# Kernel tuning notes

Hardware: AMD Instinct MI355X
Metric: run time of the kernel (lower is better)

Reference implementation:

```python
import jax, jax.numpy as jnp
import numpy as np

MODEL_DIM = 512
KEY_DIM = 64


def setup_inputs() -> dict:
    key = jax.random.key(0)
    ks = jax.random.split(key, 8)
    B, S = 4, 4096
    scale = 1.0 / np.sqrt(MODEL_DIM)
    return {
        "x1": jax.random.normal(ks[0], (B, S, MODEL_DIM), jnp.float32),
        "x2": jax.random.normal(ks[1], (B, S, MODEL_DIM), jnp.float32),
        "Wq": jax.random.normal(ks[2], (MODEL_DIM, KEY_DIM), jnp.float32) * scale,
        "bq": jnp.zeros((KEY_DIM,), jnp.float32),
        "Wk": jax.random.normal(ks[3], (MODEL_DIM, KEY_DIM), jnp.float32) * scale,
        "bk": jnp.zeros((KEY_DIM,), jnp.float32),
        "Wv": jax.random.normal(ks[4], (MODEL_DIM, KEY_DIM), jnp.float32) * scale,
        "bv": jnp.zeros((KEY_DIM,), jnp.float32),
        "apply_mask": 1,
    }


def reference(x1, x2, Wq, bq, Wk, bk, Wv, bv, apply_mask):
    # Linear + ReLU projections (single head, d_k = d_v = KEY_DIM)
    q = jax.nn.relu(x1 @ Wq + bq)  # [B,S,dk]
    k = jax.nn.relu(x2 @ Wk + bk)  # [B,S,dk]
    v = jax.nn.relu(x2 @ Wv + bv)  # [B,S,dk]
    scores = jnp.einsum("bqd,bkd->bqk", q, k) / jnp.sqrt(jnp.float32(KEY_DIM))
    if apply_mask:
        S = scores.shape[-1]
        causal = jnp.tril(jnp.ones((S, S), dtype=bool))  # keep lower-tri incl. diag
        scores = jnp.where(causal, scores, -jnp.inf)
    attn = jax.nn.softmax(scores, axis=-1)
    return jnp.einsum("bqk,bkd->bqd", attn, v)
```

## Files before the change

kernel.cpp:

```cpp
#include <hip/hip_runtime.h>


typedef __attribute__((ext_vector_type(8))) _Float16 f16x8;
typedef __attribute__((ext_vector_type(4))) float f32x4;
typedef __attribute__((ext_vector_type(8))) unsigned short us8;
typedef __attribute__((ext_vector_type(4))) unsigned short us4;

#define AS1 __attribute__((address_space(1)))
#define AS3 __attribute__((address_space(3)))

__device__ __forceinline__ void gload16(const void* g, void* l) {
  __builtin_amdgcn_global_load_lds((const AS1 unsigned int*)g,
                                   (AS3 unsigned int*)l, 16, 0, 0);
}

__device__ __forceinline__ unsigned short f2h(float f) {
  _Float16 h = (_Float16)f;
  return __builtin_bit_cast(unsigned short, h);
}
__device__ __forceinline__ float h2f(unsigned short u) {
  return (float)__builtin_bit_cast(_Float16, u);
}
__device__ __forceinline__ f16x8 us2h(us8 v) {
  return __builtin_bit_cast(f16x8, v);
}

#define S_LEN 4096
#define NROW 16384
#define CCH 8
#define NPMAX 8

__global__ __launch_bounds__(256) void prep_kernel(
    const float* __restrict__ Wq, const float* __restrict__ Wk,
    const float* __restrict__ Wv, unsigned short* __restrict__ wtT) {
  const int kc = blockIdx.x, p = blockIdx.y;
  const float* __restrict__ W = (p == 0) ? Wq : (p == 1) ? Wk : Wv;
  __shared__ unsigned short T[64][72];
  const int t = threadIdx.x;
#pragma unroll
  for (int i = 0; i < 4; i++) {
    int f = t + 256 * i;
    int kk = f >> 4, c4 = (f & 15) << 2;
    float4 v4 = *(const float4*)&W[(size_t)(kc * 64 + kk) * 64 + c4];
    T[c4 + 0][kk] = f2h(v4.x);
    T[c4 + 1][kk] = f2h(v4.y);
    T[c4 + 2][kk] = f2h(v4.z);
    T[c4 + 3][kk] = f2h(v4.w);
  }
  __syncthreads();
  const int n = t >> 2, q4 = (t & 3) << 4;
  us8 o0, o1;
#pragma unroll
  for (int e = 0; e < 8; e++) o0[e] = T[n][q4 + e];
#pragma unroll
  for (int e = 0; e < 8; e++) o1[e] = T[n][q4 + 8 + e];
  unsigned short* dst = &wtT[((size_t)p * 64 + n) * 512 + kc * 64 + q4];
  *(us8*)&dst[0] = o0;
  *(us8*)&dst[8] = o1;
}

__global__ __launch_bounds__(128) void proj_kernel(
    const float* __restrict__ x1, const float* __restrict__ x2,
    const unsigned short* __restrict__ wtT, const float* __restrict__ bq,
    const float* __restrict__ bk, const float* __restrict__ bv,
    unsigned short* __restrict__ qo, unsigned short* __restrict__ ko,
    unsigned short* __restrict__ vto) {
  const int kind = blockIdx.y;
  const float* __restrict__ X = kind ? x2 : x1;
  const int row0 = blockIdx.x * 32;

  __shared__ __align__(16) float XB[2][32 * 64];

  const int t = threadIdx.x, ln = t & 63, w = t >> 6, lm = ln & 15, lg = ln >> 4;

  f32x4 acc0[4], acc1[4];
#pragma unroll
  for (int nt = 0; nt < 4; nt++)
#pragma unroll
    for (int e = 0; e < 4; e++) { acc0[nt][e] = 0.0f; acc1[nt][e] = 0.0f; }

  const unsigned short* __restrict__ wt0 =
      wtT + (size_t)(kind ? 1 : 0) * 64 * 512;
  const unsigned short* __restrict__ wt1 = wtT + (size_t)2 * 64 * 512;

  auto STAGE = [&](int kc, int bi) {
#pragma unroll
    for (int cc = 0; cc < 4; cc++) {
      int c = 4 * w + cc;
      int r = 4 * c + (ln >> 4);
      int s = ln & 15;
      int sg = (s & 8) | ((s & 7) ^ (r & 7));
      gload16(&X[(size_t)(row0 + r) * 512 + kc * 64 + sg * 4],
              &XB[bi][c * 256]);
    }
  };

  STAGE(0, 0);
  for (int kc = 0; kc < 8; kc++) {
    const int bi = kc & 1;
    us8 B0[8], B1[8];
#pragma unroll
    for (int nt = 0; nt < 4; nt++)
#pragma unroll
      for (int h = 0; h < 2; h++)
        B0[nt * 2 + h] = *(const us8*)&wt0[(size_t)(16 * nt + lm) * 512 +
                                           kc * 64 + 32 * h + 8 * lg];
    if (kind) {
#pragma unroll
      for (int nt = 0; nt < 4; nt++)
#pragma unroll
        for (int h = 0; h < 2; h++)
          B1[nt * 2 + h] = *(const us8*)&wt1[(size_t)(16 * nt + lm) * 512 +
                                             kc * 64 + 32 * h + 8 * lg];
    }
    if (kc < 7) STAGE(kc + 1, bi ^ 1);
    if (kind) {
      if (kc < 7) asm volatile("s_waitcnt vmcnt(20)" ::: "memory");
      else        asm volatile("s_waitcnt vmcnt(16)" ::: "memory");
    } else {
      if (kc < 7) asm volatile("s_waitcnt vmcnt(12)" ::: "memory");
      else        asm volatile("s_waitcnt vmcnt(8)" ::: "memory");
    }
    __builtin_amdgcn_sched_barrier(0);
    __builtin_amdgcn_s_barrier();

    const int R = 16 * w + lm;
    f16x8 af[2];
#pragma unroll
    for (int g = 0; g < 2; g++) {
      int sl0 = 8 * g + ((2 * lg) ^ (lm & 7));
      int sl1 = 8 * g + ((2 * lg + 1) ^ (lm & 7));
      f32x4 a0 = *(const f32x4*)&XB[bi][R * 64 + sl0 * 4];
      f32x4 a1 = *(const f32x4*)&XB[bi][R * 64 + sl1 * 4];
      f16x8 v;
      v[0] = (_Float16)a0[0]; v[1] = (_Float16)a0[1];
      v[2] = (_Float16)a0[2]; v[3] = (_Float16)a0[3];
      v[4] = (_Float16)a1[0]; v[5] = (_Float16)a1[1];
      v[6] = (_Float16)a1[2]; v[7] = (_Float16)a1[3];
      af[g] = v;
    }
#pragma unroll
    for (int nt = 0; nt < 4; nt++) {
      acc0[nt] = __builtin_amdgcn_mfma_f32_16x16x32_f16(af[0], us2h(B0[nt * 2 + 0]), acc0[nt], 0, 0, 0);
      acc0[nt] = __builtin_amdgcn_mfma_f32_16x16x32_f16(af[1], us2h(B0[nt * 2 + 1]), acc0[nt], 0, 0, 0);
      if (kind) {
        acc1[nt] = __builtin_amdgcn_mfma_f32_16x16x32_f16(af[0], us2h(B1[nt * 2 + 0]), acc1[nt], 0, 0, 0);
        acc1[nt] = __builtin_amdgcn_mfma_f32_16x16x32_f16(af[1], us2h(B1[nt * 2 + 1]), acc1[nt], 0, 0, 0);
      }
    }
    __builtin_amdgcn_sched_barrier(0);
    __builtin_amdgcn_s_barrier();
  }

  if (kind == 0) {
#pragma unroll
    for (int nt = 0; nt < 4; nt++)
#pragma unroll
      for (int r = 0; r < 4; r++) {
        int row = row0 + 16 * w + 4 * lg + r;
        int col = 16 * nt + lm;
        float v = fmaxf(acc0[nt][r] + bq[col], 0.0f) * 0.125f;
        qo[(size_t)row * 64 + col] = f2h(v);
      }
  } else {
#pragma unroll
    for (int nt = 0; nt < 4; nt++)
#pragma unroll
      for (int r = 0; r < 4; r++) {
        int row = row0 + 16 * w + 4 * lg + r;
        int col = 16 * nt + lm;
        float v = fmaxf(acc0[nt][r] + bk[col], 0.0f);
        ko[(size_t)row * 64 + col] = f2h(v);
      }
    unsigned short* TB = (unsigned short*)&XB[0][0];
#pragma unroll
    for (int nt = 0; nt < 4; nt++)
#pragma unroll
      for (int r = 0; r < 4; r++) {
        float v = fmaxf(acc1[nt][r] + bv[16 * nt + lm], 0.0f);
        TB[(16 * w + 4 * lg + r) * 72 + 16 * nt + lm] = f2h(v);
      }
    __syncthreads();
    const int d = t >> 1, s0 = (t & 1) << 4;
    us8 o0, o1;
#pragma unroll
    for (int e = 0; e < 8; e++) o0[e] = TB[(s0 + e) * 72 + d];
#pragma unroll
    for (int e = 0; e < 8; e++) o1[e] = TB[(s0 + 8 + e) * 72 + d];
    const int batch = row0 >> 12, sl = row0 & 4095;
    unsigned short* vp = &vto[((size_t)batch * 64 + d) * S_LEN + sl + s0];
    *(us8*)&vp[0] = o0;
    *(us8*)&vp[8] = o1;
  }
}

__global__ __launch_bounds__(256) void attn_part(
    const unsigned short* __restrict__ q, const unsigned short* __restrict__ k,
    const unsigned short* __restrict__ vT, const int* __restrict__ amask,
    unsigned short* __restrict__ pO, float* __restrict__ pml) {
  const int qt = blockIdx.x, j = blockIdx.y, b = blockIdx.z;
  const int mask = *amask;
  const int sb = j * CCH;
  if (mask && sb > qt) return;
  const int se0 = sb + CCH - 1;
  const int se = mask ? ((qt < se0) ? qt : se0) : se0;

  const int t = threadIdx.x, ln = t & 63, w = t >> 6, lm = ln & 15, lg = ln >> 4;

  __shared__ __align__(16) unsigned short KB[2][4096];
  __shared__ __align__(16) unsigned short VB[2][4096];
  __shared__ __align__(16) unsigned short Ps[4][16][72];

  const unsigned short* __restrict__ qb = q + (size_t)b * S_LEN * 64;
  const unsigned short* __restrict__ kb = k + (size_t)b * S_LEN * 64;
  const unsigned short* __restrict__ vb = vT + (size_t)b * 64 * S_LEN;

  const size_t qoff = (size_t)(qt * 64 + 16 * w + lm) * 64;
  f16x8 qf0 = *(const f16x8*)&qb[qoff + 8 * lg];
  f16x8 qf1 = *(const f16x8*)&qb[qoff + 32 + 8 * lg];

  const int rr = ln >> 3;
  const int sg = (ln & 7) ^ (rr & 7);
  auto STAGE = [&](int s, int bi) {
    const int kv0 = s * 64;
#pragma unroll
    for (int cc = 0; cc < 2; cc++) {
      int c = 2 * w + cc;
      int r = 8 * c + rr;
      gload16(&kb[(size_t)(kv0 + r) * 64 + sg * 8], &KB[bi][c * 512]);
      gload16(&vb[(size_t)r * S_LEN + kv0 + sg * 8], &VB[bi][c * 512]);
    }
  };

  f32x4 accO[4];
#pragma unroll
  for (int dt = 0; dt < 4; dt++)
#pragma unroll
    for (int e = 0; e < 4; e++) accO[dt][e] = 0.0f;
  float m0 = -1e30f, l0 = 0.0f;

  const int sx = lm & 7;
  STAGE(sb, 0);
  for (int s = sb; s <= se; s++) {
    const int bi = (s - sb) & 1;
    if (s < se) {
      STAGE(s + 1, bi ^ 1);
      asm volatile("s_waitcnt vmcnt(4)" ::: "memory");
    } else {
      asm volatile("s_waitcnt vmcnt(0)" ::: "memory");
    }
    __builtin_amdgcn_sched_barrier(0);
    __builtin_amdgcn_s_barrier();

    f32x4 sc[4];
#pragma unroll
    for (int nt = 0; nt < 4; nt++) {
#pragma unroll
      for (int e = 0; e < 4; e++) sc[nt][e] = 0.0f;
      const int R = 16 * nt + lm;
      f16x8 kf0 = *(const f16x8*)&KB[bi][R * 64 + (lg ^ sx) * 8];
      f16x8 kf1 = *(const f16x8*)&KB[bi][R * 64 + ((4 + lg) ^ sx) * 8];
      sc[nt] = __builtin_amdgcn_mfma_f32_16x16x32_f16(kf0, qf0, sc[nt], 0, 0, 0);
      sc[nt] = __builtin_amdgcn_mfma_f32_16x16x32_f16(kf1, qf1, sc[nt], 0, 0, 0);
    }

    if (mask && s == qt) {
#pragma unroll
      for (int nt = 0; nt < 4; nt++)
#pragma unroll
        for (int r = 0; r < 4; r++)
          if (16 * nt + 4 * lg + r > 16 * w + lm) sc[nt][r] = -1e30f;
    }

    float mx = fmaxf(fmaxf(fmaxf(sc[0][0], sc[0][1]), fmaxf(sc[0][2], sc[0][3])),
                     fmaxf(fmaxf(sc[1][0], sc[1][1]), fmaxf(sc[1][2], sc[1][3])));
    float mx2 = fmaxf(fmaxf(fmaxf(sc[2][0], sc[2][1]), fmaxf(sc[2][2], sc[2][3])),
                      fmaxf(fmaxf(sc[3][0], sc[3][1]), fmaxf(sc[3][2], sc[3][3])));
    mx = fmaxf(mx, mx2);
    mx = fmaxf(mx, __shfl_xor(mx, 16));
    mx = fmaxf(mx, __shfl_xor(mx, 32));
    const float mn = fmaxf(m0, mx);
    const float fs = __expf(m0 - mn);
    m0 = mn;

    float pv[4][4];
    float su = 0.0f;
#pragma unroll
    for (int nt = 0; nt < 4; nt++)
#pragma unroll
      for (int r = 0; r < 4; r++) {
        pv[nt][r] = __expf(sc[nt][r] - mn);
        su += pv[nt][r];
      }
    su += __shfl_xor(su, 16);
    su += __shfl_xor(su, 32);
    l0 = l0 * fs + su;
#pragma unroll
    for (int dt = 0; dt < 4; dt++)
#pragma unroll
      for (int e = 0; e < 4; e++) accO[dt][e] *= fs;

#pragma unroll
    for (int nt = 0; nt < 4; nt++) {
      us4 w4;
#pragma unroll
      for (int r = 0; r < 4; r++) w4[r] = f2h(pv[nt][r]);
      *(us4*)&Ps[w][lm][16 * nt + 4 * lg] = w4;
    }

    f16x8 pf0 = *(const f16x8*)&Ps[w][lm][8 * lg];
    f16x8 pf1 = *(const f16x8*)&Ps[w][lm][32 + 8 * lg];
#pragma unroll
    for (int dt = 0; dt < 4; dt++) {
      const int R = 16 * dt + lm;
      f16x8 vf0 = *(const f16x8*)&VB[bi][R * 64 + (lg ^ sx) * 8];
      f16x8 vf1 = *(const f16x8*)&VB[bi][R * 64 + ((4 + lg) ^ sx) * 8];
      accO[dt] = __builtin_amdgcn_mfma_f32_16x16x32_f16(vf0, pf0, accO[dt], 0, 0, 0);
      accO[dt] = __builtin_amdgcn_mfma_f32_16x16x32_f16(vf1, pf1, accO[dt], 0, 0, 0);
    }
    __builtin_amdgcn_sched_barrier(0);
    __builtin_amdgcn_s_barrier();
  }

  const size_t ub = (size_t)(b * 64 + qt) * NPMAX + j;
  unsigned short* __restrict__ Op = pO + ub * 4096;
#pragma unroll
  for (int dt = 0; dt < 4; dt++) {
    us4 o4;
#pragma unroll
    for (int r = 0; r < 4; r++) o4[r] = f2h(accO[dt][r]);
    *(us4*)&Op[(16 * w + lm) * 64 + 16 * dt + 4 * lg] = o4;
  }
  if (lg == 0) {
    float* __restrict__ mlp = pml + ub * 128;
    mlp[(16 * w + lm) * 2 + 0] = m0;
    mlp[(16 * w + lm) * 2 + 1] = l0;
  }
}

__global__ __launch_bounds__(256) void combine_kernel(
    const unsigned short* __restrict__ pO, const float* __restrict__ pml,
    const int* __restrict__ amask, float* __restrict__ out) {
  const int qt = blockIdx.x, cg = blockIdx.y, b = blockIdx.z;
  const int mask = *amask;
  const int np = mask ? (qt / CCH + 1) : NPMAX;
  const int t = threadIdx.x;
  const int row = t >> 2, c = ((t & 3) << 2) + (cg << 4);
  const size_t base = (size_t)(b * 64 + qt) * NPMAX;

  float M = -1e30f;
  for (int jj = 0; jj < np; jj++)
    M = fmaxf(M, pml[(base + jj) * 128 + row * 2]);

  float L = 0.0f;
  float a[4] = {0.f, 0.f, 0.f, 0.f};
  for (int jj = 0; jj < np; jj++) {
    const float* mlp = &pml[(base + jj) * 128 + row * 2];
    float wj = __expf(mlp[0] - M);
    L += mlp[1] * wj;
    us4 h = *(const us4*)&pO[(base + jj) * 4096 + row * 64 + c];
#pragma unroll
    for (int e = 0; e < 4; e++) a[e] += wj * h2f(h[e]);
  }
  const float inv = 1.0f / L;
  f32x4 o;
#pragma unroll
  for (int e = 0; e < 4; e++) o[e] = a[e] * inv;
  *(f32x4*)&out[((size_t)b * S_LEN + qt * 64 + row) * 64 + c] = o;
}

extern "C" void kernel_launch(void* const* d_in, const int* in_sizes, int n_in,
                              void* d_out, int out_size, void* d_ws, size_t ws_size,
                              hipStream_t stream) {
  const float* x1 = (const float*)d_in[0];
  const float* x2 = (const float*)d_in[1];
  const float* Wq = (const float*)d_in[2];
  const float* bq = (const float*)d_in[3];
  const float* Wk = (const float*)d_in[4];
  const float* bk = (const float*)d_in[5];
  const float* Wv = (const float*)d_in[6];
  const float* bv = (const float*)d_in[7];
  const int* amask = (const int*)d_in[8];

  unsigned short* qws = (unsigned short*)d_ws;
  unsigned short* kws = qws + (size_t)NROW * 64;
  unsigned short* vtws = kws + (size_t)NROW * 64;
  unsigned short* wtT = vtws + (size_t)NROW * 64;
  unsigned short* pO = wtT + (size_t)3 * 64 * 512;
  float* pml = (float*)(pO + (size_t)2048 * 4096);
  float* out = (float*)d_out;

  prep_kernel<<<dim3(8, 3), 256, 0, stream>>>(Wq, Wk, Wv, wtT);
  proj_kernel<<<dim3(512, 2), 128, 0, stream>>>(x1, x2, wtT, bq, bk, bv,
                                                qws, kws, vtws);
  attn_part<<<dim3(64, NPMAX, 4), 256, 0, stream>>>(qws, kws, vtws, amask,
                                                    pO, pml);
  combine_kernel<<<dim3(64, 4, 4), 256, 0, stream>>>(pO, pml, amask, out);
}
```

Measured before the change: 165.7 us.

## Load projection inputs directly to registers and raise MFMA wave priority in attention

The projection kernel no longer stages X tiles through double-buffered LDS with async global_load_lds, explicit vmcnt waits and barriers. Each lane now reads its own row of X directly from global memory into registers, and weight fragments are loaded inline next to their MFMAs. This removes the LDS footprint and the block-wide syncs, at the cost of less latency hiding and possibly less coalesced global reads. Separately, the attention kernel wraps its QK and PV MFMA blocks in s_setprio(1) so those waves are favoured by the scheduler.

```diff
diff --git a/kernel.cpp b/kernel.cpp
--- a/kernel.cpp
+++ b/kernel.cpp
@@ -69,7 +69,7 @@
   const float* __restrict__ X = kind ? x2 : x1;
   const int row0 = blockIdx.x * 32;
 
-  __shared__ __align__(16) float XB[2][32 * 64];
+  __shared__ __align__(16) unsigned short TB[32 * 72];
 
   const int t = threadIdx.x, ln = t & 63, w = t >> 6, lm = ln & 15, lg = ln >> 4;
 
@@ -82,74 +82,37 @@
   const unsigned short* __restrict__ wt0 =
       wtT + (size_t)(kind ? 1 : 0) * 64 * 512;
   const unsigned short* __restrict__ wt1 = wtT + (size_t)2 * 64 * 512;
-
-  auto STAGE = [&](int kc, int bi) {
-#pragma unroll
-    for (int cc = 0; cc < 4; cc++) {
-      int c = 4 * w + cc;
-      int r = 4 * c + (ln >> 4);
-      int s = ln & 15;
-      int sg = (s & 8) | ((s & 7) ^ (r & 7));
-      gload16(&X[(size_t)(row0 + r) * 512 + kc * 64 + sg * 4],
-              &XB[bi][c * 256]);
-    }
-  };
-
-  STAGE(0, 0);
+  const float* __restrict__ xrow = &X[(size_t)(row0 + 16 * w + lm) * 512];
+
+#pragma unroll 2
   for (int kc = 0; kc < 8; kc++) {
-    const int bi = kc & 1;
-    us8 B0[8], B1[8];
-#pragma unroll
-    for (int nt = 0; nt < 4; nt++)
-#pragma unroll
-      for (int h = 0; h < 2; h++)
-        B0[nt * 2 + h] = *(const us8*)&wt0[(size_t)(16 * nt + lm) * 512 +
-                                           kc * 64 + 32 * h + 8 * lg];
-    if (kind) {
-#pragma unroll
-      for (int nt = 0; nt < 4; nt++)
-#pragma unroll
-        for (int h = 0; h < 2; h++)
-          B1[nt * 2 + h] = *(const us8*)&wt1[(size_t)(16 * nt + lm) * 512 +
-                                             kc * 64 + 32 * h + 8 * lg];
-    }
-    if (kc < 7) STAGE(kc + 1, bi ^ 1);
-    if (kind) {
-      if (kc < 7) asm volatile("s_waitcnt vmcnt(20)" ::: "memory");
-      else        asm volatile("s_waitcnt vmcnt(16)" ::: "memory");
-    } else {
-      if (kc < 7) asm volatile("s_waitcnt vmcnt(12)" ::: "memory");
-      else        asm volatile("s_waitcnt vmcnt(8)" ::: "memory");
-    }
-    __builtin_amdgcn_sched_barrier(0);
-    __builtin_amdgcn_s_barrier();
-
-    const int R = 16 * w + lm;
     f16x8 af[2];
 #pragma unroll
-    for (int g = 0; g < 2; g++) {
-      int sl0 = 8 * g + ((2 * lg) ^ (lm & 7));
-      int sl1 = 8 * g + ((2 * lg + 1) ^ (lm & 7));
-      f32x4 a0 = *(const f32x4*)&XB[bi][R * 64 + sl0 * 4];
-      f32x4 a1 = *(const f32x4*)&XB[bi][R * 64 + sl1 * 4];
+    for (int h = 0; h < 2; h++) {
+      const float* ap = &xrow[kc * 64 + 32 * h + 8 * lg];
+      float4 a0 = *(const float4*)ap;
+      float4 a1 = *(const float4*)(ap + 4);
       f16x8 v;
-      v[0] = (_Float16)a0[0]; v[1] = (_Float16)a0[1];
-      v[2] = (_Float16)a0[2]; v[3] = (_Float16)a0[3];
-      v[4] = (_Float16)a1[0]; v[5] = (_Float16)a1[1];
-      v[6] = (_Float16)a1[2]; v[7] = (_Float16)a1[3];
-      af[g] = v;
+      v[0] = (_Float16)a0.x; v[1] = (_Float16)a0.y;
+      v[2] = (_Float16)a0.z; v[3] = (_Float16)a0.w;
+      v[4] = (_Float16)a1.x; v[5] = (_Float16)a1.y;
+      v[6] = (_Float16)a1.z; v[7] = (_Float16)a1.w;
+      af[h] = v;
     }
 #pragma unroll
     for (int nt = 0; nt < 4; nt++) {
-      acc0[nt] = __builtin_amdgcn_mfma_f32_16x16x32_f16(af[0], us2h(B0[nt * 2 + 0]), acc0[nt], 0, 0, 0);
-      acc0[nt] = __builtin_amdgcn_mfma_f32_16x16x32_f16(af[1], us2h(B0[nt * 2 + 1]), acc0[nt], 0, 0, 0);
+      const size_t rb = (size_t)(16 * nt + lm) * 512 + kc * 64 + 8 * lg;
+      us8 b00 = *(const us8*)&wt0[rb];
+      us8 b01 = *(const us8*)&wt0[rb + 32];
+      acc0[nt] = __builtin_amdgcn_mfma_f32_16x16x32_f16(af[0], us2h(b00), acc0[nt], 0, 0, 0);
+      acc0[nt] = __builtin_amdgcn_mfma_f32_16x16x32_f16(af[1], us2h(b01), acc0[nt], 0, 0, 0);
       if (kind) {
-        acc1[nt] = __builtin_amdgcn_mfma_f32_16x16x32_f16(af[0], us2h(B1[nt * 2 + 0]), acc1[nt], 0, 0, 0);
-        acc1[nt] = __builtin_amdgcn_mfma_f32_16x16x32_f16(af[1], us2h(B1[nt * 2 + 1]), acc1[nt], 0, 0, 0);
-      }
-    }
-    __builtin_amdgcn_sched_barrier(0);
-    __builtin_amdgcn_s_barrier();
+        us8 b10 = *(const us8*)&wt1[rb];
+        us8 b11 = *(const us8*)&wt1[rb + 32];
+        acc1[nt] = __builtin_amdgcn_mfma_f32_16x16x32_f16(af[0], us2h(b10), acc1[nt], 0, 0, 0);
+        acc1[nt] = __builtin_amdgcn_mfma_f32_16x16x32_f16(af[1], us2h(b11), acc1[nt], 0, 0, 0);
+      }
+    }
   }
 
   if (kind == 0) {
@@ -172,7 +135,6 @@
         float v = fmaxf(acc0[nt][r] + bk[col], 0.0f);
         ko[(size_t)row * 64 + col] = f2h(v);
       }
-    unsigned short* TB = (unsigned short*)&XB[0][0];
 #pragma unroll
     for (int nt = 0; nt < 4; nt++)
 #pragma unroll
@@ -253,6 +215,7 @@
     __builtin_amdgcn_s_barrier();
 
     f32x4 sc[4];
+    __builtin_amdgcn_s_setprio(1);
 #pragma unroll
     for (int nt = 0; nt < 4; nt++) {
 #pragma unroll
@@ -263,6 +226,7 @@
       sc[nt] = __builtin_amdgcn_mfma_f32_16x16x32_f16(kf0, qf0, sc[nt], 0, 0, 0);
       sc[nt] = __builtin_amdgcn_mfma_f32_16x16x32_f16(kf1, qf1, sc[nt], 0, 0, 0);
     }
+    __builtin_amdgcn_s_setprio(0);
 
     if (mask && s == qt) {
 #pragma unroll
@@ -310,6 +274,7 @@
 
     f16x8 pf0 = *(const f16x8*)&Ps[w][lm][8 * lg];
     f16x8 pf1 = *(const f16x8*)&Ps[w][lm][32 + 8 * lg];
+    __builtin_amdgcn_s_setprio(1);
 #pragma unroll
     for (int dt = 0; dt < 4; dt++) {
       const int R = 16 * dt + lm;
@@ -318,6 +283,7 @@
       accO[dt] = __builtin_amdgcn_mfma_f32_16x16x32_f16(vf0, pf0, accO[dt], 0, 0, 0);
       accO[dt] = __builtin_amdgcn_mfma_f32_16x16x32_f16(vf1, pf1, accO[dt], 0, 0, 0);
     }
+    __builtin_amdgcn_s_setprio(0);
     __builtin_amdgcn_sched_barrier(0);
     __builtin_amdgcn_s_barrier();
   }
```

Result: slower. 170.9 us (+3.1%).
